# Optimization experiments

Measured on AMD Instinct MI355X. Metric: run time of the kernel, lower is better.

Reference implementation:

```python
import jax, jax.numpy as jnp
import numpy as np

B = 2097152
T = 4      # num_tokens
E = 16     # attn_embed_dim
H = 32     # hidden_dim
O = 16     # output_dim


def _xavier(key, shape):
    fan_out, fan_in = shape
    std = np.sqrt(2.0 / (fan_in + fan_out)).astype(np.float32)
    return jax.random.normal(key, shape, dtype=jnp.float32) * std


def setup_inputs() -> dict:
    key = jax.random.key(0)
    ks = jax.random.split(key, 7)
    x = jax.random.normal(ks[0], (B, 1), dtype=jnp.float32)
    # initial_fc: Linear(1 -> T*E)
    W0 = _xavier(ks[1], (T * E, 1)); b0 = jnp.zeros((T * E,), jnp.float32)
    # MultiheadAttention packed in-projection: [3E, E]
    Wqkv = _xavier(ks[2], (3 * E, E)); bqkv = jnp.zeros((3 * E,), jnp.float32)
    # out_proj: Linear(E -> E)
    Wo = _xavier(ks[3], (E, E)); bo = jnp.zeros((E,), jnp.float32)
    # post_fc: Linear(E -> H), LeakyReLU(0.01), Linear(H -> O)
    W1 = _xavier(ks[4], (H, E)); b1 = jnp.zeros((H,), jnp.float32)
    W2 = _xavier(ks[5], (O, H)); b2 = jnp.zeros((O,), jnp.float32)
    return {"x": x, "W0": W0, "b0": b0, "Wqkv": Wqkv, "bqkv": bqkv,
            "Wo": Wo, "bo": bo, "W1": W1, "b1": b1, "W2": W2, "b2": b2}


def reference(x, W0, b0, Wqkv, bqkv, Wo, bo, W1, b1, W2, b2):
    b = x.shape[0]
    scale = jnp.float32(1.0 / np.sqrt(E))
    # expand scalar -> tokens [B, T, E]
    tokens = (x @ W0.T + b0).reshape(b, T, E)
    # packed QKV projection (PyTorch MHA, 1 head)
    qkv = jnp.einsum('bte,fe->btf', tokens, Wqkv) + bqkv  # [B, T, 3E]
    q, k, v = jnp.split(qkv, 3, axis=-1)
    scores = jnp.einsum('bqe,bke->bqk', q, k) * scale     # [B, T, T]
    attn = jax.nn.softmax(scores, axis=-1)
    ctx = jnp.einsum('bqk,bke->bqe', attn, v)             # [B, T, E]
    attn_out = ctx @ Wo.T + bo
    pooled = attn_out.mean(axis=1)                        # [B, E]
    h = jax.nn.leaky_relu(pooled @ W1.T + b1, negative_slope=0.01)
    return h @ W2.T + b2                                  # [B, O]
```

## Files before the change

kernel.cpp:

```cpp
#include <hip/hip_runtime.h>
#include <hip/hip_bf16.h>


#define WS_SA 0
#define WS_SB 16
#define WS_SC 32
#define WS_A1 48
#define WS_A2 1072
#define WS_A3 1584
#define WS_BC 2096
#define WS_K8 2608

using f32x4 = __attribute__((ext_vector_type(4))) float;
using bf16x8 = __attribute__((ext_vector_type(8))) short;

union FragU {
  unsigned u[4];
  bf16x8 v;
};

__device__ inline f32x4 mfma16(bf16x8 a, bf16x8 b, f32x4 c) {
  return __builtin_amdgcn_mfma_f32_16x16x32_bf16(a, b, c, 0, 0, 0);
}

__device__ inline unsigned short bf16_rne(float f) {
  unsigned u = __float_as_uint(f);
  unsigned lsb = (u >> 16) & 1u;
  u += 0x7fffu + lsb;
  return (unsigned short)(u >> 16);
}
__device__ inline float bf16_f32(unsigned short h) {
  return __uint_as_float(((unsigned)h) << 16);
}
__device__ inline unsigned pack2(unsigned short lo, unsigned short hi) {
  return (unsigned)lo | ((unsigned)hi << 16);
}
__device__ inline unsigned cvt2(float a, float b) {
  unsigned r;
  asm("v_cvt_pk_bf16_f32 %0, %1, %2" : "=v"(r) : "v"(a), "v"(b));
  return r;
}
__device__ inline unsigned cvt2abs(float a, float b) {
  unsigned r;
  asm("v_cvt_pk_bf16_f32 %0, abs(%1), abs(%2)" : "=v"(r) : "v"(a), "v"(b));
  return r;
}
__device__ inline float lo_f32(unsigned u) { return __uint_as_float(u << 16); }
__device__ inline float hi_f32(unsigned u) {
  return __uint_as_float(u & 0xffff0000u);
}
__device__ inline float uni(float v) {
  return __int_as_float(__builtin_amdgcn_readfirstlane(__float_as_int(v)));
}

__global__ __launch_bounds__(256) void precompute_kernel(
    const float* __restrict__ W0, const float* __restrict__ b0,
    const float* __restrict__ Wqkv, const float* __restrict__ bqkv,
    const float* __restrict__ Wo, const float* __restrict__ bo,
    const float* __restrict__ W1, const float* __restrict__ b1,
    const float* __restrict__ W2, const float* __restrict__ b2,
    float* __restrict__ wsf) {
  unsigned* wsu = (unsigned*)wsf;
  __shared__ float P[4][48], Q[4][48], Wc[32][16];
  __shared__ float M[32][8], bcs[32], W2M[16][8], c8[16];
  const int tid = threadIdx.x;

  for (int idx = tid; idx < 4 * 48; idx += 256) {
    int t = idx / 48, f = idx % 48;
    float p = 0.f, q = 0.f;
    for (int e = 0; e < 16; ++e) {
      float w = Wqkv[f * 16 + e];
      p += W0[t * 16 + e] * w;
      q += b0[t * 16 + e] * w;
    }
    P[t][f] = p;
    Q[t][f] = q + bqkv[f];
  }
  for (int idx = tid; idx < 32 * 16; idx += 256) {
    int h = idx / 16, e = idx % 16;
    float acc = 0.f;
    for (int ep = 0; ep < 16; ++ep) acc += W1[h * 16 + ep] * Wo[ep * 16 + e];
    Wc[h][e] = acc;
  }
  __syncthreads();

  const float SCL = 0.25f * 1.4426950408889634f;
  for (int idx = tid; idx < 16; idx += 256) {
    int i = idx / 4, j = idx % 4;
    float a = 0.f, b = 0.f, c = 0.f;
    for (int e = 0; e < 16; ++e) {
      float pq = P[i][e], qq = Q[i][e];
      float pk = P[j][16 + e], qk = Q[j][16 + e];
      a += pq * pk;
      b += pq * qk + qq * pk;
      c += qq * qk;
    }
    wsf[WS_SA + idx] = a * SCL;
    wsf[WS_SB + idx] = b * SCL;
    wsf[WS_SC + idx] = c * SCL;
  }
  for (int idx = tid; idx < 32; idx += 256) {
    float acc = b1[idx];
    for (int ep = 0; ep < 16; ++ep) acc += W1[idx * 16 + ep] * bo[ep];
    bcs[idx] = acc;
  }
  for (int idx = tid; idx < 256; idx += 256) {
    int h = idx >> 3, k = idx & 7, j = k & 3;
    float acc = 0.f;
    if (k < 4)
      for (int e = 0; e < 16; ++e) acc += Wc[h][e] * P[j][32 + e];
    else
      for (int e = 0; e < 16; ++e) acc += Wc[h][e] * Q[j][32 + e];
    M[h][k] = 0.25f * acc;
  }
  __syncthreads();
  for (int idx = tid; idx < 128; idx += 256) {
    int o = idx >> 3, k = idx & 7;
    float acc = 0.f;
    for (int h = 0; h < 32; ++h) acc += W2[o * 32 + h] * M[h][k];
    W2M[o][k] = acc;
  }
  for (int idx = tid; idx < 16; idx += 256) {
    float acc = 0.f;
    for (int h = 0; h < 32; ++h) acc += W2[idx * 32 + h] * bcs[h];
    c8[idx] = acc;
  }
  __syncthreads();

  if (tid < 64) {
    const int lane = tid;
    const int g = lane >> 4, row = lane & 15;
    for (int hb = 0; hb < 2; ++hb) {
      int h = 16 * hb + row;
      for (int dw = 0; dw < 4; ++dw) {
        float m0 = (g == 0) ? M[h][2 * dw] : 0.f;
        float m1 = (g == 0) ? M[h][2 * dw + 1] : 0.f;
        unsigned short h0 = bf16_rne(m0), h1 = bf16_rne(m1);
        unsigned short l0 = bf16_rne(m0 - bf16_f32(h0));
        unsigned short l1 = bf16_rne(m1 - bf16_f32(h1));
        wsu[WS_A1 + ((hb * 2 + 0) * 64 + lane) * 4 + dw] = pack2(h0, h1);
        wsu[WS_A1 + ((hb * 2 + 1) * 64 + lane) * 4 + dw] = pack2(l0, l1);
      }
    }
    for (int dw = 0; dw < 4; ++dw) {
      float m0 = (g == 0) ? 0.505f * W2M[row][2 * dw] : 0.f;
      float m1 = (g == 0) ? 0.505f * W2M[row][2 * dw + 1] : 0.f;
      unsigned short h0 = bf16_rne(m0), h1 = bf16_rne(m1);
      unsigned short l0 = bf16_rne(m0 - bf16_f32(h0));
      unsigned short l1 = bf16_rne(m1 - bf16_f32(h1));
      wsu[WS_A2 + (0 * 64 + lane) * 4 + dw] = pack2(h0, h1);
      wsu[WS_A2 + (1 * 64 + lane) * 4 + dw] = pack2(l0, l1);
    }
    for (int dw = 0; dw < 4; ++dw) {
      int j0 = 2 * dw, j1 = 2 * dw + 1;
      int H0 = (j0 < 4) ? 4 * g + j0 : 16 + 4 * g + (j0 - 4);
      int H1 = (j1 < 4) ? 4 * g + j1 : 16 + 4 * g + (j1 - 4);
      float m0 = 0.495f * W2[row * 32 + H0];
      float m1 = 0.495f * W2[row * 32 + H1];
      unsigned short h0 = bf16_rne(m0), h1 = bf16_rne(m1);
      unsigned short l0 = bf16_rne(m0 - bf16_f32(h0));
      unsigned short l1 = bf16_rne(m1 - bf16_f32(h1));
      wsu[WS_A3 + (0 * 64 + lane) * 4 + dw] = pack2(h0, h1);
      wsu[WS_A3 + (1 * 64 + lane) * 4 + dw] = pack2(l0, l1);
    }
    for (int hb = 0; hb < 2; ++hb)
      for (int r = 0; r < 4; ++r)
        wsf[WS_BC + lane * 8 + hb * 4 + r] = bcs[16 * hb + 4 * g + r];
    for (int r = 0; r < 4; ++r)
      wsf[WS_K8 + lane * 4 + r] = 0.505f * c8[4 * g + r] + b2[4 * g + r];
  }
}

__global__ __launch_bounds__(256, 4) void subnet_mfma_kernel(
    const float* __restrict__ x, const float* __restrict__ wsf,
    float* __restrict__ out, int B) {
  const unsigned* wsu = (const unsigned*)wsf;
  const int lane = threadIdx.x & 63;
  const int wave = blockIdx.x * (blockDim.x >> 6) + (threadIdx.x >> 6);
  const int g = lane >> 4;

  FragU A1h0, A1l0, A1h1, A1l1, A2h, A2l, A3h, A3l;
#pragma unroll
  for (int dw = 0; dw < 4; ++dw) {
    A1h0.u[dw] = wsu[WS_A1 + ((0) * 64 + lane) * 4 + dw];
    A1l0.u[dw] = wsu[WS_A1 + ((1) * 64 + lane) * 4 + dw];
    A1h1.u[dw] = wsu[WS_A1 + ((2) * 64 + lane) * 4 + dw];
    A1l1.u[dw] = wsu[WS_A1 + ((3) * 64 + lane) * 4 + dw];
    A2h.u[dw] = wsu[WS_A2 + (0 * 64 + lane) * 4 + dw];
    A2l.u[dw] = wsu[WS_A2 + (1 * 64 + lane) * 4 + dw];
    A3h.u[dw] = wsu[WS_A3 + (0 * 64 + lane) * 4 + dw];
    A3l.u[dw] = wsu[WS_A3 + (1 * 64 + lane) * 4 + dw];
  }
  f32x4 bc0, bc1, k8;
#pragma unroll
  for (int r = 0; r < 4; ++r) {
    bc0[r] = wsf[WS_BC + lane * 8 + r];
    bc1[r] = wsf[WS_BC + lane * 8 + 4 + r];
    k8[r] = wsf[WS_K8 + lane * 4 + r];
  }
  float sa[16], sb[16], sc[16];
#pragma unroll
  for (int i = 0; i < 16; ++i) {
    sa[i] = uni(wsf[WS_SA + i]);
    sb[i] = wsf[WS_SB + i];
    sc[i] = uni(wsf[WS_SC + i]);
  }
  const int permidx = (lane & 15) * 4;
  const long nchunk = (long)(B >> 6);

  const float* xp = x + (long)wave * 256 + lane;
  float xs4[4];
#pragma unroll
  for (int ci = 0; ci < 4; ++ci) {
    const long chunk = (long)wave * 4 + ci;
    xs4[ci] = (chunk < nchunk) ? __builtin_nontemporal_load(xp + ci * 64) : 0.f;
  }

  float* op = out + ((long)wave * 256 + (lane & 15)) * 16 + 4 * g;

#pragma unroll 1
  for (int ci = 0; ci < 4; ++ci) {
    const long chunk = (long)wave * 4 + ci;
    if (chunk >= nchunk) break;
    const float xx = xs4[ci];

    float s0 = 0.f, s1 = 0.f, s2 = 0.f, s3 = 0.f;
#pragma unroll
    for (int i = 0; i < 4; ++i) {
      float r0 = (sa[i * 4 + 0] * xx + sb[i * 4 + 0]) * xx + sc[i * 4 + 0];
      float r1 = (sa[i * 4 + 1] * xx + sb[i * 4 + 1]) * xx + sc[i * 4 + 1];
      float r2 = (sa[i * 4 + 2] * xx + sb[i * 4 + 2]) * xx + sc[i * 4 + 2];
      float r3 = (sa[i * 4 + 3] * xx + sb[i * 4 + 3]) * xx + sc[i * 4 + 3];
      float p0 = __builtin_amdgcn_exp2f(r0);
      float p1 = __builtin_amdgcn_exp2f(r1);
      float p2 = __builtin_amdgcn_exp2f(r2);
      float p3 = __builtin_amdgcn_exp2f(r3);
      float rinv = __builtin_amdgcn_rcpf(p0 + p1 + p2 + p3);
      s0 += p0 * rinv;
      s1 += p1 * rinv;
      s2 += p2 * rinv;
      s3 += p3 * rinv;
    }

    float gv[8] = {xx * s0, xx * s1, xx * s2, xx * s3, s0, s1, s2, s3};
    unsigned gh[4], gl[4];
#pragma unroll
    for (int d = 0; d < 4; ++d) {
      unsigned ph = cvt2(gv[2 * d], gv[2 * d + 1]);
      gh[d] = ph;
      gl[d] = cvt2(gv[2 * d] - lo_f32(ph), gv[2 * d + 1] - hi_f32(ph));
    }

#pragma unroll
    for (int eg = 0; eg < 4; ++eg) {
      const int pidx = permidx + 64 * eg;
      FragU Bh, Bl;
#pragma unroll
      for (int d = 0; d < 4; ++d) {
        Bh.u[d] = (unsigned)__builtin_amdgcn_ds_bpermute(pidx, (int)gh[d]);
        Bl.u[d] = (unsigned)__builtin_amdgcn_ds_bpermute(pidx, (int)gl[d]);
      }
      f32x4 z0 = bc0, z1 = bc1;
      z0 = mfma16(A1h0.v, Bh.v, z0);
      z1 = mfma16(A1h1.v, Bh.v, z1);
      z0 = mfma16(A1l0.v, Bh.v, z0);
      z1 = mfma16(A1l1.v, Bh.v, z1);
      z0 = mfma16(A1h0.v, Bl.v, z0);
      z1 = mfma16(A1h1.v, Bl.v, z1);
      float zz[8];
      zz[0] = z0[0]; zz[1] = z0[1]; zz[2] = z0[2]; zz[3] = z0[3];
      zz[4] = z1[0]; zz[5] = z1[1]; zz[6] = z1[2]; zz[7] = z1[3];
      FragU Zh, Zl;
#pragma unroll
      for (int d = 0; d < 4; ++d) {
        unsigned ph = cvt2abs(zz[2 * d], zz[2 * d + 1]);
        Zh.u[d] = ph;
        Zl.u[d] = cvt2(fabsf(zz[2 * d]) - lo_f32(ph),
                       fabsf(zz[2 * d + 1]) - hi_f32(ph));
      }
      f32x4 acc = k8;
      acc = mfma16(A3h.v, Zh.v, acc);
      acc = mfma16(A3l.v, Zh.v, acc);
      acc = mfma16(A3h.v, Zl.v, acc);
      acc = mfma16(A2h.v, Bh.v, acc);
      acc = mfma16(A2l.v, Bh.v, acc);
      acc = mfma16(A2h.v, Bl.v, acc);
      *reinterpret_cast<f32x4*>(op + eg * 256) = acc;
    }
    op += 1024;
  }
}

extern "C" void kernel_launch(void* const* d_in, const int* in_sizes, int n_in,
                              void* d_out, int out_size, void* d_ws,
                              size_t ws_size, hipStream_t stream) {
  const float* x = (const float*)d_in[0];
  const float* W0 = (const float*)d_in[1];
  const float* b0 = (const float*)d_in[2];
  const float* Wqkv = (const float*)d_in[3];
  const float* bqkv = (const float*)d_in[4];
  const float* Wo = (const float*)d_in[5];
  const float* bo = (const float*)d_in[6];
  const float* W1 = (const float*)d_in[7];
  const float* b1 = (const float*)d_in[8];
  const float* W2 = (const float*)d_in[9];
  const float* b2 = (const float*)d_in[10];
  float* out = (float*)d_out;
  float* ws = (float*)d_ws;

  const int B = in_sizes[0];

  precompute_kernel<<<1, 256, 0, stream>>>(W0, b0, Wqkv, bqkv, Wo, bo, W1, b1,
                                           W2, b2, ws);

  const int blocks = (B + 1023) / 1024;
  subnet_mfma_kernel<<<blocks, 256, 0, stream>>>(x, ws, out, B);
}
```

Measured before the change: 44.98 us.

## Pack hi/lo bf16 split terms into the unused K lanes of single MFMAs

The first-layer and skip-path MFMAs previously issued three separate 16x16x32 instructions (hi*hi, lo*hi, hi*lo) with only 8 of 32 K entries populated. The weight fragments now place hi, lo, hi and zero in the four K groups, and the B operand selects hi or lo per group, so one MFMA computes all three split products. This cuts six MFMAs to two on the A1 path and three to one on the A2 path, and also drops the min-waves launch bound and uses nontemporal output stores. It relies on the K-group-to-lane mapping being exactly right, and removing the occupancy hint may change register allocation.

```diff
diff --git a/kernel.cpp b/kernel.cpp
--- a/kernel.cpp
+++ b/kernel.cpp
@@ -6,10 +6,10 @@
 #define WS_SB 16
 #define WS_SC 32
 #define WS_A1 48
-#define WS_A2 1072
-#define WS_A3 1584
-#define WS_BC 2096
-#define WS_K8 2608
+#define WS_A2 560
+#define WS_A3 816
+#define WS_BC 1328
+#define WS_K8 1840
 
 using f32x4 = __attribute__((ext_vector_type(4))) float;
 using bf16x8 = __attribute__((ext_vector_type(8))) short;
@@ -129,32 +129,34 @@
 
   if (tid < 64) {
     const int lane = tid;
-    const int g = lane >> 4, row = lane & 15;
+    const int gg = lane >> 4, row = lane & 15;
     for (int hb = 0; hb < 2; ++hb) {
       int h = 16 * hb + row;
       for (int dw = 0; dw < 4; ++dw) {
-        float m0 = (g == 0) ? M[h][2 * dw] : 0.f;
-        float m1 = (g == 0) ? M[h][2 * dw + 1] : 0.f;
+        float m0 = M[h][2 * dw];
+        float m1 = M[h][2 * dw + 1];
         unsigned short h0 = bf16_rne(m0), h1 = bf16_rne(m1);
         unsigned short l0 = bf16_rne(m0 - bf16_f32(h0));
         unsigned short l1 = bf16_rne(m1 - bf16_f32(h1));
-        wsu[WS_A1 + ((hb * 2 + 0) * 64 + lane) * 4 + dw] = pack2(h0, h1);
-        wsu[WS_A1 + ((hb * 2 + 1) * 64 + lane) * 4 + dw] = pack2(l0, l1);
+        unsigned hi = pack2(h0, h1), lo = pack2(l0, l1);
+        unsigned val = (gg == 1) ? lo : ((gg == 3) ? 0u : hi);
+        wsu[WS_A1 + (hb * 64 + lane) * 4 + dw] = val;
       }
     }
     for (int dw = 0; dw < 4; ++dw) {
-      float m0 = (g == 0) ? 0.505f * W2M[row][2 * dw] : 0.f;
-      float m1 = (g == 0) ? 0.505f * W2M[row][2 * dw + 1] : 0.f;
+      float m0 = 0.505f * W2M[row][2 * dw];
+      float m1 = 0.505f * W2M[row][2 * dw + 1];
       unsigned short h0 = bf16_rne(m0), h1 = bf16_rne(m1);
       unsigned short l0 = bf16_rne(m0 - bf16_f32(h0));
       unsigned short l1 = bf16_rne(m1 - bf16_f32(h1));
-      wsu[WS_A2 + (0 * 64 + lane) * 4 + dw] = pack2(h0, h1);
-      wsu[WS_A2 + (1 * 64 + lane) * 4 + dw] = pack2(l0, l1);
+      unsigned hi = pack2(h0, h1), lo = pack2(l0, l1);
+      unsigned val = (gg == 1) ? lo : ((gg == 3) ? 0u : hi);
+      wsu[WS_A2 + lane * 4 + dw] = val;
     }
     for (int dw = 0; dw < 4; ++dw) {
       int j0 = 2 * dw, j1 = 2 * dw + 1;
-      int H0 = (j0 < 4) ? 4 * g + j0 : 16 + 4 * g + (j0 - 4);
-      int H1 = (j1 < 4) ? 4 * g + j1 : 16 + 4 * g + (j1 - 4);
+      int H0 = (j0 < 4) ? 4 * gg + j0 : 16 + 4 * gg + (j0 - 4);
+      int H1 = (j1 < 4) ? 4 * gg + j1 : 16 + 4 * gg + (j1 - 4);
       float m0 = 0.495f * W2[row * 32 + H0];
       float m1 = 0.495f * W2[row * 32 + H1];
       unsigned short h0 = bf16_rne(m0), h1 = bf16_rne(m1);
@@ -165,13 +167,13 @@
     }
     for (int hb = 0; hb < 2; ++hb)
       for (int r = 0; r < 4; ++r)
-        wsf[WS_BC + lane * 8 + hb * 4 + r] = bcs[16 * hb + 4 * g + r];
+        wsf[WS_BC + lane * 8 + hb * 4 + r] = bcs[16 * hb + 4 * gg + r];
     for (int r = 0; r < 4; ++r)
-      wsf[WS_K8 + lane * 4 + r] = 0.505f * c8[4 * g + r] + b2[4 * g + r];
-  }
-}
-
-__global__ __launch_bounds__(256, 4) void subnet_mfma_kernel(
+      wsf[WS_K8 + lane * 4 + r] = 0.505f * c8[4 * gg + r] + b2[4 * gg + r];
+  }
+}
+
+__global__ __launch_bounds__(256) void subnet_mfma_kernel(
     const float* __restrict__ x, const float* __restrict__ wsf,
     float* __restrict__ out, int B) {
   const unsigned* wsu = (const unsigned*)wsf;
@@ -179,15 +181,12 @@
   const int wave = blockIdx.x * (blockDim.x >> 6) + (threadIdx.x >> 6);
   const int g = lane >> 4;
 
-  FragU A1h0, A1l0, A1h1, A1l1, A2h, A2l, A3h, A3l;
+  FragU A1f0, A1f1, A2f, A3h, A3l;
 #pragma unroll
   for (int dw = 0; dw < 4; ++dw) {
-    A1h0.u[dw] = wsu[WS_A1 + ((0) * 64 + lane) * 4 + dw];
-    A1l0.u[dw] = wsu[WS_A1 + ((1) * 64 + lane) * 4 + dw];
-    A1h1.u[dw] = wsu[WS_A1 + ((2) * 64 + lane) * 4 + dw];
-    A1l1.u[dw] = wsu[WS_A1 + ((3) * 64 + lane) * 4 + dw];
-    A2h.u[dw] = wsu[WS_A2 + (0 * 64 + lane) * 4 + dw];
-    A2l.u[dw] = wsu[WS_A2 + (1 * 64 + lane) * 4 + dw];
+    A1f0.u[dw] = wsu[WS_A1 + (0 * 64 + lane) * 4 + dw];
+    A1f1.u[dw] = wsu[WS_A1 + (1 * 64 + lane) * 4 + dw];
+    A2f.u[dw] = wsu[WS_A2 + lane * 4 + dw];
     A3h.u[dw] = wsu[WS_A3 + (0 * 64 + lane) * 4 + dw];
     A3l.u[dw] = wsu[WS_A3 + (1 * 64 + lane) * 4 + dw];
   }
@@ -206,6 +205,7 @@
     sc[i] = uni(wsf[WS_SC + i]);
   }
   const int permidx = (lane & 15) * 4;
+  const bool useLo = (g >= 2);
   const long nchunk = (long)(B >> 6);
 
   const float* xp = x + (long)wave * 256 + lane;
@@ -254,19 +254,15 @@
 #pragma unroll
     for (int eg = 0; eg < 4; ++eg) {
       const int pidx = permidx + 64 * eg;
-      FragU Bh, Bl;
+      FragU Bf;
 #pragma unroll
       for (int d = 0; d < 4; ++d) {
-        Bh.u[d] = (unsigned)__builtin_amdgcn_ds_bpermute(pidx, (int)gh[d]);
-        Bl.u[d] = (unsigned)__builtin_amdgcn_ds_bpermute(pidx, (int)gl[d]);
+        int bh = __builtin_amdgcn_ds_bpermute(pidx, (int)gh[d]);
+        int bl = __builtin_amdgcn_ds_bpermute(pidx, (int)gl[d]);
+        Bf.u[d] = (unsigned)(useLo ? bl : bh);
       }
-      f32x4 z0 = bc0, z1 = bc1;
-      z0 = mfma16(A1h0.v, Bh.v, z0);
-      z1 = mfma16(A1h1.v, Bh.v, z1);
-      z0 = mfma16(A1l0.v, Bh.v, z0);
-      z1 = mfma16(A1l1.v, Bh.v, z1);
-      z0 = mfma16(A1h0.v, Bl.v, z0);
-      z1 = mfma16(A1h1.v, Bl.v, z1);
+      f32x4 z0 = mfma16(A1f0.v, Bf.v, bc0);
+      f32x4 z1 = mfma16(A1f1.v, Bf.v, bc1);
       float zz[8];
       zz[0] = z0[0]; zz[1] = z0[1]; zz[2] = z0[2]; zz[3] = z0[3];
       zz[4] = z1[0]; zz[5] = z1[1]; zz[6] = z1[2]; zz[7] = z1[3];
@@ -278,14 +274,12 @@
         Zl.u[d] = cvt2(fabsf(zz[2 * d]) - lo_f32(ph),
                        fabsf(zz[2 * d + 1]) - hi_f32(ph));
       }
-      f32x4 acc = k8;
+      f32x4 acc = mfma16(A2f.v, Bf.v, k8);
       acc = mfma16(A3h.v, Zh.v, acc);
       acc = mfma16(A3l.v, Zh.v, acc);
       acc = mfma16(A3h.v, Zl.v, acc);
-      acc = mfma16(A2h.v, Bh.v, acc);
-      acc = mfma16(A2l.v, Bh.v, acc);
-      acc = mfma16(A2h.v, Bl.v, acc);
-      *reinterpret_cast<f32x4*>(op + eg * 256) = acc;
+      __builtin_nontemporal_store(acc,
+                                  reinterpret_cast<f32x4*>(op + eg * 256));
     }
     op += 1024;
   }
```

Result: faster. 40.97 us (-8.9%).
